# Kernel optimization log

Measured on AMD Instinct MI355X. Metric: run time of the kernel, lower is better.

Reference implementation:

```python
import jax, jax.numpy as jnp
import numpy as np

B, C, H, W = 32, 256, 60, 60
E, O, K = 3, 256, 3          # num_experts, out_channels, kernel_size
SQ = 16                      # squeeze_channels = max(C//16, 16)
PAD, STRIDE = 1, 1
DN = ('NCHW', 'OIHW', 'NCHW')

# ---- bicubic 3->5 interpolation matrix (PyTorch bicubic, a=-0.75, align_corners=False) ----
def _cubic(t, a=-0.75):
    t = abs(t)
    if t <= 1.0:
        return (a + 2) * t**3 - (a + 3) * t**2 + 1
    if t < 2.0:
        return a * t**3 - 5 * a * t**2 + 8 * a * t - 4 * a
    return 0.0

def _bicubic_mat(n_in=3, n_out=5):
    M = np.zeros((n_out, n_in), np.float32)
    s = n_in / n_out
    for o in range(n_out):
        x = (o + 0.5) * s - 0.5
        x0 = int(np.floor(x)); f = x - x0
        for j in range(-1, 3):  # 4-tap cubic, indices clamped (border replicate)
            M[o, min(max(x0 + j, 0), n_in - 1)] += _cubic(f - j)
    return M

BICUBIC_M = jnp.asarray(_bicubic_mat())

def _pool(x, k):
    # exact PyTorch AdaptiveAvgPool2d when H,W divisible by k (true for H=W=60)
    b, c, h, w = x.shape
    return x.reshape(b, c, k, h // k, k, w // k).mean((3, 5))

def _conv(x, w, groups=1, pad=0, stride=1):
    return jax.lax.conv_general_dilated(x, w, (stride, stride), [(pad, pad)] * 2,
                                         dimension_numbers=DN, feature_group_count=groups)

def setup_inputs() -> dict:
    key = jax.random.key(0)
    ks = jax.random.split(key, 6)
    x = jax.random.normal(ks[0], (B, C, H, W), jnp.float32)
    w_expert = jax.random.normal(ks[1], (E, O, C, K, K), jnp.float32) / np.sqrt(C * K * K)
    rw1  = jax.random.normal(ks[2], (SQ, 3 * C, 1, 1), jnp.float32) / np.sqrt(3 * C)
    rdw1 = jax.random.normal(ks[3], (SQ, 1, 3, 3), jnp.float32) / 3.0
    rdw2 = jax.random.normal(ks[4], (SQ, 1, 3, 3), jnp.float32) / 3.0
    rw2  = jax.random.normal(ks[5], (E * C, SQ, 1, 1), jnp.float32) / np.sqrt(SQ)
    return {"x": x, "w_expert": w_expert, "rw1": rw1, "rdw1": rdw1, "rdw2": rdw2, "rw2": rw2}

def reference(x, w_expert, rw1, rdw1, rdw2, rw2):
    b = x.shape[0]
    # --- routing function (mode 'A') ---
    a1 = jnp.broadcast_to(_pool(x, 1), (b, C, 5, 5))          # gap1 expanded to 5x5
    p3 = _pool(x, 3)
    M = BICUBIC_M
    a3 = jnp.einsum('oi,bcij,pj->bcop', M, p3, M)             # bicubic 3x3 -> 5x5
    a5 = _pool(x, 5)
    att = jnp.concatenate([a1, a3, a5], axis=1)               # (b, 3C, 5, 5)
    h = jax.nn.relu(_conv(att, rw1))                          # (b, SQ, 5, 5)
    h = jax.nn.relu(_conv(h, rdw1, groups=SQ))                # (b, SQ, 3, 3)
    h = jax.nn.relu(_conv(h, rdw2, groups=SQ))                # (b, SQ, 1, 1)
    r = jax.nn.sigmoid(_conv(h, rw2)).reshape(b, E, C)        # (b, E, C)
    # --- combine expert kernels per sample, apply per-sample conv ---
    cw = jnp.einsum('bec,eockl->bockl', r, w_expert)          # (b, O, C, K, K)
    y = jax.vmap(lambda xi, wi: _conv(xi[None], wi, pad=PAD, stride=STRIDE)[0])(x, cw)
    return y
```

## Files before the change

kernel.cpp:

```cpp
#include <hip/hip_runtime.h>

typedef unsigned short u16;
typedef unsigned int u32;
typedef __attribute__((ext_vector_type(8))) short bfrag;
typedef __attribute__((ext_vector_type(16))) float f32x16;

#define GAS __attribute__((address_space(1)))
#define LAS __attribute__((address_space(3)))

__device__ __forceinline__ u16 f2bf(float f) {
  u32 u = __builtin_bit_cast(u32, f);
  u = (u + 0x7fffu + ((u >> 16) & 1u)) >> 16;
  return (u16)u;
}
__device__ __forceinline__ float bf2f(u16 b) {
  u32 u = ((u32)b) << 16;
  return __builtin_bit_cast(float, u);
}

__device__ __forceinline__ void glds16(const u16* src, u16* dst) {
  __builtin_amdgcn_global_load_lds((const GAS unsigned int*)src,
                                   (LAS unsigned int*)dst, 16, 0, 0);
}

__device__ __constant__ float Mb[5][3] = {
  { 1.096f, -0.096f,  0.0f  },
  { 0.612f,  0.46f,  -0.072f},
  { 0.0f,    1.0f,    0.0f  },
  {-0.072f,  0.46f,   0.612f},
  { 0.0f,   -0.096f,  1.096f},
};

__global__ __launch_bounds__(256) void att_kernel(const float* __restrict__ x,
                                                  float* __restrict__ att) {
  int bc = blockIdx.x;
  int b = bc >> 8, c = bc & 255;
  const float* xc = x + (size_t)bc * 3600;
  __shared__ float s15[225];
  __shared__ float p3s[9];
  int t = threadIdx.x;
  if (t < 225) {
    int i = t / 15, j = t - (t / 15) * 15;
    const float* base = xc + i * 4 * 60 + j * 4;
    float s = 0.f;
#pragma unroll
    for (int r = 0; r < 4; ++r) {
      float4 v = *reinterpret_cast<const float4*>(base + r * 60);
      s += v.x + v.y + v.z + v.w;
    }
    s15[t] = s;
  }
  __syncthreads();
  float a5v = 0.f;
  if (t < 25) {
    int ii = t / 5, jj = t - (t / 5) * 5;
    float s = 0.f;
#pragma unroll
    for (int r = 0; r < 3; ++r)
#pragma unroll
      for (int cc = 0; cc < 3; ++cc) s += s15[(ii * 3 + r) * 15 + jj * 3 + cc];
    a5v = s * (1.f / 144.f);
  }
  if (t >= 64 && t < 73) {
    int i3 = t - 64;
    int pi = i3 / 3, pj = i3 - pi * 3;
    float s = 0.f;
#pragma unroll
    for (int r = 0; r < 5; ++r)
#pragma unroll
      for (int cc = 0; cc < 5; ++cc) s += s15[(pi * 5 + r) * 15 + pj * 5 + cc];
    p3s[i3] = s * (1.f / 400.f);
  }
  __syncthreads();
  float* attb = att + (size_t)b * 768 * 25;
  if (t < 25) {
    attb[(512 + c) * 25 + t] = a5v;
    int o = t / 5, qq = t - (t / 5) * 5;
    float s = 0.f;
#pragma unroll
    for (int i = 0; i < 3; ++i) {
      float mi = Mb[o][i];
#pragma unroll
      for (int j = 0; j < 3; ++j) s += mi * Mb[qq][j] * p3s[i * 3 + j];
    }
    attb[(256 + c) * 25 + t] = s;
  } else if (t == 32) {
    float s = 0.f;
#pragma unroll
    for (int i = 0; i < 9; ++i) s += p3s[i];
    s *= (1.f / 9.f);
    for (int p = 0; p < 25; ++p) attb[c * 25 + p] = s;
  }
}

__global__ __launch_bounds__(256) void route_kernel(
    const float* __restrict__ att, const float* __restrict__ rw1,
    const float* __restrict__ rdw1, const float* __restrict__ rdw2,
    const float* __restrict__ rw2, float* __restrict__ rout) {
  int b = blockIdx.x;
  int t = threadIdx.x;
  __shared__ u16 attS[768 * 25];
  __shared__ float h1[16 * 25];
  __shared__ float h2[16 * 9];
  __shared__ float h3[16];
  const float* attb = att + (size_t)b * 768 * 25;
  for (int i = t; i < 768 * 25; i += 256) attS[i] = f2bf(attb[i]);
  __syncthreads();
  for (int idx = t; idx < 400; idx += 256) {
    int sq = idx / 25, p = idx - (idx / 25) * 25;
    const float* wrow = rw1 + sq * 768;
    float s = 0.f;
    for (int ic = 0; ic < 768; ++ic) s += wrow[ic] * bf2f(attS[ic * 25 + p]);
    h1[idx] = fmaxf(s, 0.f);
  }
  __syncthreads();
  for (int idx = t; idx < 144; idx += 256) {
    int sq = idx / 9, ij = idx - (idx / 9) * 9;
    int i = ij / 3, j = ij - (ij / 3) * 3;
    float s = 0.f;
#pragma unroll
    for (int u = 0; u < 3; ++u)
#pragma unroll
      for (int v = 0; v < 3; ++v)
        s += rdw1[sq * 9 + u * 3 + v] * h1[sq * 25 + (i + u) * 5 + (j + v)];
    h2[idx] = fmaxf(s, 0.f);
  }
  __syncthreads();
  if (t < 16) {
    float s = 0.f;
#pragma unroll
    for (int uv = 0; uv < 9; ++uv) s += rdw2[t * 9 + uv] * h2[t * 9 + uv];
    h3[t] = fmaxf(s, 0.f);
  }
  __syncthreads();
  for (int idx = t; idx < 768; idx += 256) {
    float s = 0.f;
#pragma unroll
    for (int sq = 0; sq < 16; ++sq) s += rw2[idx * 16 + sq] * h3[sq];
    rout[(size_t)b * 768 + idx] = 1.f / (1.f + expf(-s));
  }
}

__global__ __launch_bounds__(256) void cw_kernel(const float* __restrict__ rout,
                                                 const float* __restrict__ we,
                                                 u16* __restrict__ cw) {
  int idx = blockIdx.x * 256 + threadIdx.x;
  if (idx >= 32 * 256 * 256) return;
  int b = idx >> 16;
  int oc = idx & 65535;
  int o = oc >> 8, c = oc & 255;
  float r0 = rout[b * 768 + c];
  float r1 = rout[b * 768 + 256 + c];
  float r2 = rout[b * 768 + 512 + c];
  const size_t ES = (size_t)256 * 256 * 9;
  const float* w0 = we + ((size_t)o * 256 + c) * 9;
  int ctile = c >> 6, c_loc = c & 63;
  u16* dst = cw + ((size_t)(b * 256 + o)) * 2304 + ctile * 576 + c_loc;
#pragma unroll
  for (int tp = 0; tp < 9; ++tp) {
    float f = r0 * w0[tp] + r1 * w0[ES + tp] + r2 * w0[2 * ES + tp];
    dst[tp * 64] = f2bf(f);
  }
}

__global__ __launch_bounds__(256) void xprep_kernel(const float* __restrict__ x,
                                                    u16* __restrict__ xpad) {
  const int row = blockIdx.x;
  const int b = blockIdx.y;
  const int t = threadIdx.x;
  u16* outrow = xpad + ((size_t)(b * 62 + row)) * 64 * 256;
  if (row == 0 || row == 61) {
    uint4 z = {0, 0, 0, 0};
#pragma unroll
    for (int i = 0; i < 8; ++i)
      *reinterpret_cast<uint4*>(outrow + (size_t)(t + i * 256) * 8) = z;
    return;
  }
  const int h = row - 1;
  __shared__ float xs[64 * 62];
  const float* xb = x + ((size_t)b * 256) * 3600 + h * 60;
  for (int cc = 0; cc < 4; ++cc) {
    for (int u = t; u < 960; u += 256) {
      int c = u / 15, seg = u - (u / 15) * 15;
      float4 v = *reinterpret_cast<const float4*>(xb + (size_t)(cc * 64 + c) * 3600 + seg * 4);
      float* d = &xs[c * 62 + seg * 4];
      d[0] = v.x; d[1] = v.y; d[2] = v.z; d[3] = v.w;
    }
    __syncthreads();
    for (int u = t; u < 512; u += 256) {
      int col = u >> 3, slot = u & 7;
      uint4 o = {0, 0, 0, 0};
      if (col >= 1 && col <= 60) {
        int w = col - 1;
        u16 tmp[8];
#pragma unroll
        for (int j = 0; j < 8; ++j) tmp[j] = f2bf(xs[(slot * 8 + j) * 62 + w]);
        o = *reinterpret_cast<uint4*>(tmp);
      }
      *reinterpret_cast<uint4*>(outrow + (size_t)col * 256 + cc * 64 + slot * 8) = o;
    }
    __syncthreads();
  }
}

__global__ __launch_bounds__(512, 2) void conv_kernel(const u16* __restrict__ xpad,
                                                      const u16* __restrict__ cw,
                                                      float* __restrict__ y) {
  __shared__ __align__(16) u16 smem[57344];

  const int flat = blockIdx.x;
  const int wg = (flat & 7) * 60 + (flat >> 3);
  const int b = wg / 15;
  const int rg = wg - b * 15;
  const int h0 = rg * 4;

  const int t = threadIdx.x;
  const int wave = t >> 6, lane = t & 63;
  const int wm = wave >> 2, wn = wave & 3;
  const int r32 = lane & 31, half = lane >> 5, l7 = lane & 7;

  const u16* cwB = cw + (size_t)b * 256 * 2304;
  const u16* xpB = xpad + ((size_t)(b * 62 + h0) * 64) * 256;

  int a_src[4], a_du[4];
#pragma unroll
  for (int i = 0; i < 4; ++i) {
    int u = i * 512 + t;
    int m = u >> 3, sd = u & 7, ss = sd ^ (m & 7);
    a_src[i] = m * 2304 + ss * 8;
    a_du[i] = u * 8;
  }
  int x_src[6], x_du[6];
#pragma unroll
  for (int i = 0; i < 6; ++i) {
    int u = i * 512 + t;
    int row = u >> 9, col = (u >> 3) & 63, sd = u & 7, ss = sd ^ (col & 7);
    x_src[i] = (row * 64 + col) * 256 + ss * 8;
    x_du[i] = u * 8;
  }

  const int abase = wm * 8192 + r32 * 64 + ((half ^ l7) * 8);
  int bcb[3];
#pragma unroll
  for (int kw = 0; kw < 3; ++kw) {
    int rk = r32 + kw;
    bcb[kw] = rk * 64 + ((half ^ (rk & 7)) * 8);
  }

  f32x16 acc[4][2] = {};

  auto stageA = [&](int koff, int bufsel) {
    u16* dst = smem + 24576 + bufsel * 16384;
#pragma unroll
    for (int i = 0; i < 4; ++i) glds16(cwB + a_src[i] + koff, dst + a_du[i]);
  };
  auto stageX = [&](int ct) {
#pragma unroll
    for (int i = 0; i < 6; ++i) glds16(xpB + x_src[i] + ct * 64, smem + x_du[i]);
  };

  stageX(0);
  stageA(0, 0);
  __syncthreads();

  for (int ct = 0; ct < 4; ++ct) {
#pragma unroll
    for (int tap = 0; tap < 9; ++tap) {
      const int cur = (ct * 9 + tap) & 1;
      const bool last = (ct == 3 && tap == 8);
      if (!last) stageA((ct * 9 + tap + 1) * 64, cur ^ 1);
      {
        const int kh = tap / 3, kw = tap - kh * 3;
        const u16* Ab = smem + 24576 + cur * 16384;
        const int bb_base = (wn + kh) * 4096 + bcb[kw];
#pragma unroll
        for (int kg = 0; kg < 4; ++kg) {
          const int kx = kg << 4;
          bfrag a[4], bb[2];
#pragma unroll
          for (int mf = 0; mf < 4; ++mf)
            a[mf] = *reinterpret_cast<const bfrag*>(Ab + ((abase + mf * 2048) ^ kx));
#pragma unroll
          for (int nf = 0; nf < 2; ++nf)
            bb[nf] = *reinterpret_cast<const bfrag*>(smem + ((bb_base + nf * 2048) ^ kx));
#pragma unroll
          for (int mf = 0; mf < 4; ++mf)
#pragma unroll
            for (int nf = 0; nf < 2; ++nf)
              acc[mf][nf] = __builtin_amdgcn_mfma_f32_32x32x16_bf16(a[mf], bb[nf], acc[mf][nf], 0, 0, 0);
        }
      }
      __syncthreads();
      if (tap == 8 && ct < 3) { stageX(ct + 1); __syncthreads(); }
    }
  }

  float* yB = y + ((size_t)(b * 256 + wm * 128)) * 3600 + (size_t)(h0 + wn) * 60;
#pragma unroll
  for (int mf = 0; mf < 4; ++mf)
#pragma unroll
    for (int nf = 0; nf < 2; ++nf) {
      int w = nf * 32 + r32;
      if (w < 60) {
#pragma unroll
        for (int g = 0; g < 4; ++g)
#pragma unroll
          for (int rr = 0; rr < 4; ++rr) {
            int o_loc = mf * 32 + g * 8 + half * 4 + rr;
            yB[(size_t)o_loc * 3600 + w] = acc[mf][nf][g * 4 + rr];
          }
      }
    }
}

extern "C" void kernel_launch(void* const* d_in, const int* in_sizes, int n_in,
                              void* d_out, int out_size, void* d_ws, size_t ws_size,
                              hipStream_t stream) {
  const float* x    = (const float*)d_in[0];
  const float* we   = (const float*)d_in[1];
  const float* rw1  = (const float*)d_in[2];
  const float* rdw1 = (const float*)d_in[3];
  const float* rdw2 = (const float*)d_in[4];
  const float* rw2  = (const float*)d_in[5];
  float* y = (float*)d_out;

  char* ws = (char*)d_ws;
  float* att  = (float*)ws;
  float* rout = (float*)(ws + 2457600);
  u16*   cwp  = (u16*)(ws + 2555904);
  u16*   xpad = (u16*)(ws + 40304640);

  xprep_kernel<<<dim3(62, 32), 256, 0, stream>>>(x, xpad);
  att_kernel<<<8192, 256, 0, stream>>>(x, att);
  route_kernel<<<32, 256, 0, stream>>>(att, rw1, rdw1, rdw2, rw2, rout);
  cw_kernel<<<8192, 256, 0, stream>>>(rout, we, cwp);
  conv_kernel<<<480, 512, 0, stream>>>(xpad, cwp, y);
  (void)in_sizes; (void)n_in; (void)out_size; (void)ws_size;
}
```

Measured before the change: 250.6 us.

## Load conv weights directly from global memory and double-buffer input tiles; fuse prep kernels

The conv kernel stops staging the per-sample weight tiles through shared memory. Each wave now reads its A fragments straight from global memory (relying on cache), which removes a barrier after every tap. The input tile is double-buffered across channel tiles instead, so synchronisation drops to one barrier per channel tile. Separately, the xpad-prep and attention-pooling kernels are merged into one launch. The risk is that uncoalesced global loads on the MFMA critical path add latency that LDS staging used to hide.

```diff
diff --git a/kernel.cpp b/kernel.cpp
--- a/kernel.cpp
+++ b/kernel.cpp
@@ -31,14 +31,54 @@
   { 0.0f,   -0.096f,  1.096f},
 };
 
-__global__ __launch_bounds__(256) void att_kernel(const float* __restrict__ x,
-                                                  float* __restrict__ att) {
-  int bc = blockIdx.x;
+__global__ __launch_bounds__(256) void prep_kernel(const float* __restrict__ x,
+                                                   u16* __restrict__ xpad,
+                                                   float* __restrict__ att) {
+  const int bid = blockIdx.x;
+  const int t = threadIdx.x;
+  if (bid < 1984) {
+    const int row = bid % 62;
+    const int b = bid / 62;
+    u16* outrow = xpad + ((size_t)(b * 62 + row)) * 64 * 256;
+    if (row == 0 || row == 61) {
+      uint4 z = {0, 0, 0, 0};
+#pragma unroll
+      for (int i = 0; i < 8; ++i)
+        *reinterpret_cast<uint4*>(outrow + (size_t)(t + i * 256) * 8) = z;
+      return;
+    }
+    const int h = row - 1;
+    __shared__ float xs[64 * 62];
+    const float* xb = x + ((size_t)b * 256) * 3600 + h * 60;
+    for (int cc = 0; cc < 4; ++cc) {
+      for (int u = t; u < 960; u += 256) {
+        int c = u / 15, seg = u - (u / 15) * 15;
+        float4 v = *reinterpret_cast<const float4*>(xb + (size_t)(cc * 64 + c) * 3600 + seg * 4);
+        float* d = &xs[c * 62 + seg * 4];
+        d[0] = v.x; d[1] = v.y; d[2] = v.z; d[3] = v.w;
+      }
+      __syncthreads();
+      for (int u = t; u < 512; u += 256) {
+        int col = u >> 3, slot = u & 7;
+        uint4 o = {0, 0, 0, 0};
+        if (col >= 1 && col <= 60) {
+          int w = col - 1;
+          u16 tmp[8];
+#pragma unroll
+          for (int j = 0; j < 8; ++j) tmp[j] = f2bf(xs[(slot * 8 + j) * 62 + w]);
+          o = *reinterpret_cast<uint4*>(tmp);
+        }
+        *reinterpret_cast<uint4*>(outrow + (size_t)col * 256 + cc * 64 + slot * 8) = o;
+      }
+      __syncthreads();
+    }
+    return;
+  }
+  int bc = bid - 1984;
   int b = bc >> 8, c = bc & 255;
   const float* xc = x + (size_t)bc * 3600;
   __shared__ float s15[225];
   __shared__ float p3s[9];
-  int t = threadIdx.x;
   if (t < 225) {
     int i = t / 15, j = t - (t / 15) * 15;
     const float* base = xc + i * 4 * 60 + j * 4;
@@ -163,50 +203,10 @@
   }
 }
 
-__global__ __launch_bounds__(256) void xprep_kernel(const float* __restrict__ x,
-                                                    u16* __restrict__ xpad) {
-  const int row = blockIdx.x;
-  const int b = blockIdx.y;
-  const int t = threadIdx.x;
-  u16* outrow = xpad + ((size_t)(b * 62 + row)) * 64 * 256;
-  if (row == 0 || row == 61) {
-    uint4 z = {0, 0, 0, 0};
-#pragma unroll
-    for (int i = 0; i < 8; ++i)
-      *reinterpret_cast<uint4*>(outrow + (size_t)(t + i * 256) * 8) = z;
-    return;
-  }
-  const int h = row - 1;
-  __shared__ float xs[64 * 62];
-  const float* xb = x + ((size_t)b * 256) * 3600 + h * 60;
-  for (int cc = 0; cc < 4; ++cc) {
-    for (int u = t; u < 960; u += 256) {
-      int c = u / 15, seg = u - (u / 15) * 15;
-      float4 v = *reinterpret_cast<const float4*>(xb + (size_t)(cc * 64 + c) * 3600 + seg * 4);
-      float* d = &xs[c * 62 + seg * 4];
-      d[0] = v.x; d[1] = v.y; d[2] = v.z; d[3] = v.w;
-    }
-    __syncthreads();
-    for (int u = t; u < 512; u += 256) {
-      int col = u >> 3, slot = u & 7;
-      uint4 o = {0, 0, 0, 0};
-      if (col >= 1 && col <= 60) {
-        int w = col - 1;
-        u16 tmp[8];
-#pragma unroll
-        for (int j = 0; j < 8; ++j) tmp[j] = f2bf(xs[(slot * 8 + j) * 62 + w]);
-        o = *reinterpret_cast<uint4*>(tmp);
-      }
-      *reinterpret_cast<uint4*>(outrow + (size_t)col * 256 + cc * 64 + slot * 8) = o;
-    }
-    __syncthreads();
-  }
-}
-
 __global__ __launch_bounds__(512, 2) void conv_kernel(const u16* __restrict__ xpad,
                                                       const u16* __restrict__ cw,
                                                       float* __restrict__ y) {
-  __shared__ __align__(16) u16 smem[57344];
+  __shared__ __align__(16) u16 smem[49152];
 
   const int flat = blockIdx.x;
   const int wg = (flat & 7) * 60 + (flat >> 3);
@@ -217,19 +217,11 @@
   const int t = threadIdx.x;
   const int wave = t >> 6, lane = t & 63;
   const int wm = wave >> 2, wn = wave & 3;
-  const int r32 = lane & 31, half = lane >> 5, l7 = lane & 7;
-
-  const u16* cwB = cw + (size_t)b * 256 * 2304;
+  const int r32 = lane & 31, half = lane >> 5;
+
   const u16* xpB = xpad + ((size_t)(b * 62 + h0) * 64) * 256;
-
-  int a_src[4], a_du[4];
-#pragma unroll
-  for (int i = 0; i < 4; ++i) {
-    int u = i * 512 + t;
-    int m = u >> 3, sd = u & 7, ss = sd ^ (m & 7);
-    a_src[i] = m * 2304 + ss * 8;
-    a_du[i] = u * 8;
-  }
+  const u16* aBase = cw + ((size_t)(b * 256 + wm * 128 + r32)) * 2304 + half * 8;
+
   int x_src[6], x_du[6];
 #pragma unroll
   for (int i = 0; i < 6; ++i) {
@@ -239,7 +231,6 @@
     x_du[i] = u * 8;
   }
 
-  const int abase = wm * 8192 + r32 * 64 + ((half ^ l7) * 8);
   int bcb[3];
 #pragma unroll
   for (int kw = 0; kw < 3; ++kw) {
@@ -249,49 +240,39 @@
 
   f32x16 acc[4][2] = {};
 
-  auto stageA = [&](int koff, int bufsel) {
-    u16* dst = smem + 24576 + bufsel * 16384;
-#pragma unroll
-    for (int i = 0; i < 4; ++i) glds16(cwB + a_src[i] + koff, dst + a_du[i]);
+  auto stageX = [&](int ct, int bufsel) {
+    u16* dst = smem + bufsel * 24576;
+#pragma unroll
+    for (int i = 0; i < 6; ++i) glds16(xpB + x_src[i] + ct * 64, dst + x_du[i]);
   };
-  auto stageX = [&](int ct) {
-#pragma unroll
-    for (int i = 0; i < 6; ++i) glds16(xpB + x_src[i] + ct * 64, smem + x_du[i]);
-  };
-
-  stageX(0);
-  stageA(0, 0);
-  __syncthreads();
+
+  stageX(0, 0);
 
   for (int ct = 0; ct < 4; ++ct) {
-#pragma unroll
+    __syncthreads();
+    if (ct < 3) stageX(ct + 1, (ct + 1) & 1);
+    const u16* xs = smem + (ct & 1) * 24576;
+    const int kbase = ct * 576;
     for (int tap = 0; tap < 9; ++tap) {
-      const int cur = (ct * 9 + tap) & 1;
-      const bool last = (ct == 3 && tap == 8);
-      if (!last) stageA((ct * 9 + tap + 1) * 64, cur ^ 1);
-      {
-        const int kh = tap / 3, kw = tap - kh * 3;
-        const u16* Ab = smem + 24576 + cur * 16384;
-        const int bb_base = (wn + kh) * 4096 + bcb[kw];
-#pragma unroll
-        for (int kg = 0; kg < 4; ++kg) {
-          const int kx = kg << 4;
-          bfrag a[4], bb[2];
-#pragma unroll
-          for (int mf = 0; mf < 4; ++mf)
-            a[mf] = *reinterpret_cast<const bfrag*>(Ab + ((abase + mf * 2048) ^ kx));
+      const int kh = tap / 3, kw = tap - kh * 3;
+      const int bb_base = (wn + kh) * 4096 + bcb[kw];
+      const int koff = kbase + tap * 64;
+#pragma unroll
+      for (int kg = 0; kg < 4; ++kg) {
+        const int kx = kg << 4;
+        bfrag a[4], bb[2];
+#pragma unroll
+        for (int mf = 0; mf < 4; ++mf)
+          a[mf] = *reinterpret_cast<const bfrag*>(aBase + (size_t)mf * 73728 + koff + kg * 16);
+#pragma unroll
+        for (int nf = 0; nf < 2; ++nf)
+          bb[nf] = *reinterpret_cast<const bfrag*>(xs + ((bb_base + nf * 2048) ^ kx));
+#pragma unroll
+        for (int mf = 0; mf < 4; ++mf)
 #pragma unroll
           for (int nf = 0; nf < 2; ++nf)
-            bb[nf] = *reinterpret_cast<const bfrag*>(smem + ((bb_base + nf * 2048) ^ kx));
-#pragma unroll
-          for (int mf = 0; mf < 4; ++mf)
-#pragma unroll
-            for (int nf = 0; nf < 2; ++nf)
-              acc[mf][nf] = __builtin_amdgcn_mfma_f32_32x32x16_bf16(a[mf], bb[nf], acc[mf][nf], 0, 0, 0);
-        }
+            acc[mf][nf] = __builtin_amdgcn_mfma_f32_32x32x16_bf16(a[mf], bb[nf], acc[mf][nf], 0, 0, 0);
       }
-      __syncthreads();
-      if (tap == 8 && ct < 3) { stageX(ct + 1); __syncthreads(); }
     }
   }
 
@@ -330,8 +311,7 @@
   u16*   cwp  = (u16*)(ws + 2555904);
   u16*   xpad = (u16*)(ws + 40304640);
 
-  xprep_kernel<<<dim3(62, 32), 256, 0, stream>>>(x, xpad);
-  att_kernel<<<8192, 256, 0, stream>>>(x, att);
+  prep_kernel<<<10176, 256, 0, stream>>>(x, xpad, att);
   route_kernel<<<32, 256, 0, stream>>>(att, rw1, rdw1, rdw2, rw2, rout);
   cw_kernel<<<8192, 256, 0, stream>>>(rout, we, cwp);
   conv_kernel<<<480, 512, 0, stream>>>(xpad, cwp, y);
```

New measurement: 404.3 us. 1.61x slower.
